# Optimization experiments

Hardware: AMD Instinct MI355X
Metric: run time of the kernel (lower is better)

The kernel has to match this reference:

```python
import jax, jax.numpy as jnp
import numpy as np
from jax import lax

SEQ_LEN = 64
B, H, E, V = 32, 512, 256, 32000


def setup_inputs() -> dict:
    key = jax.random.key(0)
    ks = jax.random.split(key, 8)
    return {
        "y0": jax.random.randint(ks[0], (B,), 0, V, dtype=jnp.int32),
        "h0": jax.random.normal(ks[1], (1, B, H), dtype=jnp.float32),
        "c0": jax.random.normal(ks[2], (1, B, H), dtype=jnp.float32),
        "emb": jax.random.normal(ks[3], (V, E), dtype=jnp.float32) * 0.02,
        "W_ih": jax.random.normal(ks[4], (4 * H, E + H), dtype=jnp.float32) * 0.02,
        "W_hh": jax.random.normal(ks[5], (4 * H, H), dtype=jnp.float32) * 0.02,
        "b_ih": jnp.zeros((4 * H,), dtype=jnp.float32),
        "b_hh": jnp.zeros((4 * H,), dtype=jnp.float32),
        "W_out": jax.random.normal(ks[6], (V, 2 * H + E), dtype=jnp.float32) * 0.02,
        "b_out": jnp.zeros((V,), dtype=jnp.float32),
    }


def reference(y0, h0, c0, emb, W_ih, W_hh, b_ih, b_hh, W_out, b_out):
    z = h0[0]  # (B, H) latent, reused at every step

    def step(carry, _):
        y, h, c = carry
        y_embed = emb[y]                                   # (B, E) embedding gather
        x = jnp.concatenate([z, y_embed], axis=1)          # (B, H+E)
        gates = x @ W_ih.T + b_ih + h @ W_hh.T + b_hh      # (B, 4H)
        i, f, g, o = jnp.split(gates, 4, axis=1)           # torch LSTM gate order
        i = jax.nn.sigmoid(i)
        f = jax.nn.sigmoid(f)
        g = jnp.tanh(g)
        o = jax.nn.sigmoid(o)
        c = f * c + i * g
        h = o * jnp.tanh(c)
        feat = jnp.concatenate([z, y_embed, h], axis=1)    # (B, 2H+E)
        logits = feat @ W_out.T + b_out                    # (B, V)
        y_next = jnp.argmax(logits, axis=-1).astype(jnp.int32)
        return (y_next, h, c), logits

    (_, _, _), logits = lax.scan(step, (y0, h0[0], c0[0]), None, length=SEQ_LEN)
    # logits: (T, B, V) -> torch.stack(outputs, dim=2) gives (B, V, T)
    return jnp.transpose(logits, (1, 2, 0))
```

## Files before the change

### kernel.cpp

```cpp
#include <hip/hip_runtime.h>
#include <cstdint>
#include <cstddef>

#define BB 32
#define HH 512
#define EE 256
#define VV 32000
#define TT 64
#define KDIM 1280
#define NBLK_V 500
#define WREG 2304
#define WTS  68

__device__ __forceinline__ float sigf(float x) { return 1.0f / (1.0f + expf(-x)); }

__global__ __launch_bounds__(256) void k_init(const float* __restrict__ h0,
                                              const float* __restrict__ c0,
                                              float* __restrict__ fA,
                                              float* __restrict__ fB,
                                              float* __restrict__ cA) {
    int idx = blockIdx.x * 256 + threadIdx.x;
    int kk = idx >> 5;
    int b  = idx & 31;
    float zv = h0[b * HH + kk];
    fA[kk * BB + b] = zv;
    fB[kk * BB + b] = zv;
    fA[(768 + kk) * BB + b] = zv;
    fB[(768 + kk) * BB + b] = zv;
    cA[b * HH + kk] = c0[b * HH + kk];
}

__global__ __launch_bounds__(256) void k_pre(const float* __restrict__ Wih,
                                             const float* __restrict__ bih,
                                             const float* __restrict__ bhh,
                                             const float* __restrict__ fz,
                                             float* __restrict__ gzT) {
    __shared__ float lds[4 * WREG];
    const int tid = threadIdx.x;
    const int l = tid & 63;
    const int wu = tid >> 6;
    const int j0 = blockIdx.x * 64;
    const int js = l & 15;
    const int bg = l >> 4;
    float* R = &lds[wu * WREG];

    float acc[4][8];
#pragma unroll
    for (int i = 0; i < 4; ++i)
#pragma unroll
        for (int q = 0; q < 8; ++q) acc[i][q] = 0.f;

    for (int ch = 0; ch < 4; ++ch) {
        int kg0 = wu * 128 + ch * 32;
#pragma unroll
        for (int i = 0; i < 8; ++i) {
            int f4 = i * 64 + l;
            int r = f4 >> 3;
            int c4 = (f4 & 7) * 4;
            float4 w = *(const float4*)&Wih[(size_t)(j0 + r) * 768 + kg0 + c4];
            R[(c4 + 0) * WTS + r] = w.x;
            R[(c4 + 1) * WTS + r] = w.y;
            R[(c4 + 2) * WTS + r] = w.z;
            R[(c4 + 3) * WTS + r] = w.w;
        }
#pragma unroll 4
        for (int kk = 0; kk < 32; ++kk) {
            float4 wv = *(const float4*)&R[kk * WTS + js * 4];
            const float* fp = &fz[(kg0 + kk) * BB + bg * 8];
            float4 fa = *(const float4*)fp;
            float4 fb = *(const float4*)(fp + 4);
            float w4[4] = {wv.x, wv.y, wv.z, wv.w};
            float f8[8] = {fa.x, fa.y, fa.z, fa.w, fb.x, fb.y, fb.z, fb.w};
#pragma unroll
            for (int i = 0; i < 4; ++i)
#pragma unroll
                for (int q = 0; q < 8; ++q) acc[i][q] = fmaf(w4[i], f8[q], acc[i][q]);
        }
    }
#pragma unroll
    for (int i = 0; i < 4; ++i) {
        int r = js * 4 + i;
        *(float4*)&R[r * 36 + bg * 8] = make_float4(acc[i][0], acc[i][1], acc[i][2], acc[i][3]);
        *(float4*)&R[r * 36 + bg * 8 + 4] = make_float4(acc[i][4], acc[i][5], acc[i][6], acc[i][7]);
    }
    __syncthreads();
    {
        int j = tid >> 2;
        int bq = (tid & 3) * 8;
        float bias = bih[j0 + j] + bhh[j0 + j];
#pragma unroll
        for (int q = 0; q < 8; ++q) {
            float s = lds[0 * WREG + j * 36 + bq + q] + lds[1 * WREG + j * 36 + bq + q] +
                      lds[2 * WREG + j * 36 + bq + q] + lds[3 * WREG + j * 36 + bq + q];
            gzT[(size_t)(j0 + j) * BB + bq + q] = s + bias;
        }
    }
}

__global__ __launch_bounds__(256) void k_prelog(
    const float* __restrict__ Wout, const float* __restrict__ bout,
    const float* __restrict__ fz, float* __restrict__ lzT) {
    __shared__ float lds[4 * WREG];
    const int tid = threadIdx.x;
    const int l = tid & 63;
    const int wu = tid >> 6;
    const int v0 = blockIdx.x * 64;
    const int vs = l & 15;
    const int bg = l >> 4;
    float* R = &lds[wu * WREG];

    float acc[4][8];
#pragma unroll
    for (int i = 0; i < 4; ++i)
#pragma unroll
        for (int q = 0; q < 8; ++q) acc[i][q] = 0.f;

    for (int ch = 0; ch < 4; ++ch) {
        int kg0 = wu * 128 + ch * 32;
#pragma unroll
        for (int i = 0; i < 8; ++i) {
            int f4 = i * 64 + l;
            int r = f4 >> 3;
            int c4 = (f4 & 7) * 4;
            float4 w = *(const float4*)&Wout[(size_t)(v0 + r) * KDIM + kg0 + c4];
            R[(c4 + 0) * WTS + r] = w.x;
            R[(c4 + 1) * WTS + r] = w.y;
            R[(c4 + 2) * WTS + r] = w.z;
            R[(c4 + 3) * WTS + r] = w.w;
        }
#pragma unroll 4
        for (int kk = 0; kk < 32; ++kk) {
            float4 wv = *(const float4*)&R[kk * WTS + vs * 4];
            const float* fp = &fz[(kg0 + kk) * BB + bg * 8];
            float4 fa = *(const float4*)fp;
            float4 fb = *(const float4*)(fp + 4);
            float w4[4] = {wv.x, wv.y, wv.z, wv.w};
            float f8[8] = {fa.x, fa.y, fa.z, fa.w, fb.x, fb.y, fb.z, fb.w};
#pragma unroll
            for (int i = 0; i < 4; ++i)
#pragma unroll
                for (int q = 0; q < 8; ++q) acc[i][q] = fmaf(w4[i], f8[q], acc[i][q]);
        }
    }
#pragma unroll
    for (int i = 0; i < 4; ++i) {
        int r = vs * 4 + i;
        *(float4*)&R[r * 36 + bg * 8] = make_float4(acc[i][0], acc[i][1], acc[i][2], acc[i][3]);
        *(float4*)&R[r * 36 + bg * 8 + 4] = make_float4(acc[i][4], acc[i][5], acc[i][6], acc[i][7]);
    }
    __syncthreads();
    {
        int b = tid >> 3;
        int rg = tid & 7;
#pragma unroll
        for (int i = 0; i < 8; ++i) {
            int r = i * 8 + rg;
            float s = lds[0 * WREG + r * 36 + b] + lds[1 * WREG + r * 36 + b] +
                      lds[2 * WREG + r * 36 + b] + lds[3 * WREG + r * 36 + b] +
                      bout[v0 + r];
            lzT[(size_t)(v0 + r) * BB + b] = s;
        }
    }
}

__global__ __launch_bounds__(256) void k_gates(
    int t, const int* __restrict__ y0, const float* __restrict__ emb,
    const float* __restrict__ Wih, const float* __restrict__ Whh,
    const float* __restrict__ gzT,
    const float* __restrict__ fCur, float* __restrict__ fNext,
    const float* __restrict__ cCur, float* __restrict__ cNext,
    const float* __restrict__ apv, const int* __restrict__ api) {
    __shared__ float lds[4 * WREG];
    const int tid = threadIdx.x;
    const int l = tid & 63;
    const int wu = tid >> 6;
    const int uc = blockIdx.x >> 2;
    const int bg4 = blockIdx.x & 3;
    const int b0 = bg4 * 8;
    const int js = l & 7;
    const int bg = l >> 3;
    const int rr = l >> 3;
    const int c4s = (l & 7) * 4;

    int yv0, yv1, yv2, yv3, yv4, yv5, yv6, yv7;
    if (t == 0) {
        yv0 = y0[b0 + 0]; yv1 = y0[b0 + 1]; yv2 = y0[b0 + 2]; yv3 = y0[b0 + 3];
        yv4 = y0[b0 + 4]; yv5 = y0[b0 + 5]; yv6 = y0[b0 + 6]; yv7 = y0[b0 + 7];
    } else {
        int bi = l >> 3;
        int e0 = l & 7;
        float best = -3.4e38f;
        int bidx = 0x7fffffff;
#pragma unroll 8
        for (int it = 0; it < 63; ++it) {
            int e = e0 + it * 8;
            if (e < NBLK_V) {
                float v = apv[(b0 + bi) * NBLK_V + e];
                int ix = api[(b0 + bi) * NBLK_V + e];
                if (v > best || (v == best && ix < bidx)) { best = v; bidx = ix; }
            }
        }
#pragma unroll
        for (int d = 1; d < 8; d <<= 1) {
            float ov = __shfl_xor(best, d, 8);
            int oi = __shfl_xor(bidx, d, 8);
            if (ov > best || (ov == best && oi < bidx)) { best = ov; bidx = oi; }
        }
        yv0 = __builtin_amdgcn_readlane(bidx, 0);
        yv1 = __builtin_amdgcn_readlane(bidx, 8);
        yv2 = __builtin_amdgcn_readlane(bidx, 16);
        yv3 = __builtin_amdgcn_readlane(bidx, 24);
        yv4 = __builtin_amdgcn_readlane(bidx, 32);
        yv5 = __builtin_amdgcn_readlane(bidx, 40);
        yv6 = __builtin_amdgcn_readlane(bidx, 48);
        yv7 = __builtin_amdgcn_readlane(bidx, 56);
    }
    int yA = (bg == 0) ? yv0 : (bg == 1) ? yv1 : (bg == 2) ? yv2 : (bg == 3) ? yv3
           : (bg == 4) ? yv4 : (bg == 5) ? yv5 : (bg == 6) ? yv6 : yv7;
    const float* embA = emb + (size_t)yA * EE;

    float acc[4];
#pragma unroll
    for (int i = 0; i < 4; ++i) acc[i] = 0.f;
    float* R = &lds[wu * WREG];

    float4 pw[4];
    {
        int kgp = wu * 192;
#pragma unroll
        for (int i = 0; i < 4; ++i) {
            int r = i * 8 + rr;
            int j = uc * 8 + (r & 7) + 512 * (r >> 3);
            pw[i] = (kgp < 256)
                ? *(const float4*)&Wih[(size_t)j * 768 + 512 + kgp + c4s]
                : *(const float4*)&Whh[(size_t)j * 512 + (kgp - 256) + c4s];
        }
    }

    for (int ch = 0; ch < 6; ++ch) {
        int kg0 = wu * 192 + ch * 32;
#pragma unroll
        for (int i = 0; i < 4; ++i) {
            int r = i * 8 + rr;
            R[(c4s + 0) * WTS + r] = pw[i].x;
            R[(c4s + 1) * WTS + r] = pw[i].y;
            R[(c4s + 2) * WTS + r] = pw[i].z;
            R[(c4s + 3) * WTS + r] = pw[i].w;
        }
        if (ch < 5) {
            int kg1 = kg0 + 32;
#pragma unroll
            for (int i = 0; i < 4; ++i) {
                int r = i * 8 + rr;
                int j = uc * 8 + (r & 7) + 512 * (r >> 3);
                pw[i] = (kg1 < 256)
                    ? *(const float4*)&Wih[(size_t)j * 768 + 512 + kg1 + c4s]
                    : *(const float4*)&Whh[(size_t)j * 512 + (kg1 - 256) + c4s];
            }
        }
        if (kg0 < 256) {
#pragma unroll 4
            for (int kk = 0; kk < 32; ++kk) {
                float4 wv = *(const float4*)&R[kk * WTS + js * 4];
                float f0 = embA[kg0 + kk];
                acc[0] = fmaf(wv.x, f0, acc[0]);
                acc[1] = fmaf(wv.y, f0, acc[1]);
                acc[2] = fmaf(wv.z, f0, acc[2]);
                acc[3] = fmaf(wv.w, f0, acc[3]);
            }
        } else {
#pragma unroll 4
            for (int kk = 0; kk < 32; ++kk) {
                float4 wv = *(const float4*)&R[kk * WTS + js * 4];
                float hv = fCur[(768 + kg0 - 256 + kk) * BB + b0 + bg];
                acc[0] = fmaf(wv.x, hv, acc[0]);
                acc[1] = fmaf(wv.y, hv, acc[1]);
                acc[2] = fmaf(wv.z, hv, acc[2]);
                acc[3] = fmaf(wv.w, hv, acc[3]);
            }
        }
    }
#pragma unroll
    for (int i = 0; i < 4; ++i) {
        int r = js * 4 + i;
        R[r * 9 + bg] = acc[i];
    }
    __syncthreads();

    if (tid < 64) {
        int u = tid & 7;
        int bl = tid >> 3;
        float pre[4];
#pragma unroll
        for (int g = 0; g < 4; ++g) {
            int r = u + 8 * g;
            float s = lds[0 * WREG + r * 9 + bl] + lds[1 * WREG + r * 9 + bl] +
                      lds[2 * WREG + r * 9 + bl] + lds[3 * WREG + r * 9 + bl];
            int j = uc * 8 + u + 512 * g;
            pre[g] = s + gzT[(size_t)j * BB + b0 + bl];
        }
        float ig = sigf(pre[0]);
        float fg = sigf(pre[1]);
        float gg = tanhf(pre[2]);
        float og = sigf(pre[3]);
        int u_g = uc * 8 + u;
        int b = b0 + bl;
        float cp = cCur[b * HH + u_g];
        float cn = fg * cp + ig * gg;
        float hn = og * tanhf(cn);
        cNext[b * HH + u_g] = cn;
        fNext[(768 + u_g) * BB + b] = hn;
    }
    if (uc == 0) {
        int yv[8] = {yv0, yv1, yv2, yv3, yv4, yv5, yv6, yv7};
#pragma unroll
        for (int i = 0; i < 8; ++i)
            fNext[(512 + tid) * BB + b0 + i] = emb[(size_t)yv[i] * EE + tid];
    }
}

__global__ __launch_bounds__(512, 4) void k_logits(
    int t, const float* __restrict__ Wout, const float* __restrict__ lzT,
    const float* __restrict__ feat, float* __restrict__ outbuf, int direct,
    float* __restrict__ apv, int* __restrict__ api) {
    __shared__ float lds[8 * WREG];
    const int tid = threadIdx.x;
    const int l = tid & 63;
    const int wu = tid >> 6;
    const int v0 = blockIdx.x * 64;
    const int vs = l & 15;
    const int bg = l >> 4;
    const int rr = l >> 3;
    const int c4s = (l & 7) * 4;
    float* R = &lds[wu * WREG];

    float acc[4][8];
#pragma unroll
    for (int i = 0; i < 4; ++i)
#pragma unroll
        for (int q = 0; q < 8; ++q) acc[i][q] = 0.f;

    float4 pw[8];
    {
        int kgp = wu * 96;
#pragma unroll
        for (int i = 0; i < 8; ++i)
            pw[i] = *(const float4*)&Wout[(size_t)(v0 + i * 8 + rr) * KDIM + 512 + kgp + c4s];
    }

    for (int ch = 0; ch < 3; ++ch) {
        int kg0 = wu * 96 + ch * 32;
#pragma unroll
        for (int i = 0; i < 8; ++i) {
            int r = i * 8 + rr;
            R[(c4s + 0) * WTS + r] = pw[i].x;
            R[(c4s + 1) * WTS + r] = pw[i].y;
            R[(c4s + 2) * WTS + r] = pw[i].z;
            R[(c4s + 3) * WTS + r] = pw[i].w;
        }
        if (ch < 2) {
            int kg1 = kg0 + 32;
#pragma unroll
            for (int i = 0; i < 8; ++i)
                pw[i] = *(const float4*)&Wout[(size_t)(v0 + i * 8 + rr) * KDIM + 512 + kg1 + c4s];
        }
#pragma unroll 4
        for (int kk = 0; kk < 32; ++kk) {
            float4 wv = *(const float4*)&R[kk * WTS + vs * 4];
            const float* fp = &feat[(512 + kg0 + kk) * BB + bg * 8];
            float4 fa = *(const float4*)fp;
            float4 fb = *(const float4*)(fp + 4);
            float w4[4] = {wv.x, wv.y, wv.z, wv.w};
            float f8[8] = {fa.x, fa.y, fa.z, fa.w, fb.x, fb.y, fb.z, fb.w};
#pragma unroll
            for (int i = 0; i < 4; ++i)
#pragma unroll
                for (int q = 0; q < 8; ++q) acc[i][q] = fmaf(w4[i], f8[q], acc[i][q]);
        }
    }
#pragma unroll
    for (int i = 0; i < 4; ++i) {
        int r = vs * 4 + i;
        *(float4*)&R[r * 36 + bg * 8] = make_float4(acc[i][0], acc[i][1], acc[i][2], acc[i][3]);
        *(float4*)&R[r * 36 + bg * 8 + 4] = make_float4(acc[i][4], acc[i][5], acc[i][6], acc[i][7]);
    }
    __syncthreads();

    {
        int b = tid >> 4;
        int rg = tid & 15;
        float best = -3.4e38f;
        int bidx = 0x7fffffff;
#pragma unroll
        for (int i = 0; i < 4; ++i) {
            int r = i * 16 + rg;
            float s = lds[0 * WREG + r * 36 + b] + lds[1 * WREG + r * 36 + b] +
                      lds[2 * WREG + r * 36 + b] + lds[3 * WREG + r * 36 + b] +
                      lds[4 * WREG + r * 36 + b] + lds[5 * WREG + r * 36 + b] +
                      lds[6 * WREG + r * 36 + b] + lds[7 * WREG + r * 36 + b] +
                      lzT[(size_t)(v0 + r) * BB + b];
            if (!direct)
                outbuf[((size_t)t * BB + b) * VV + v0 + r] = s;
            else
                outbuf[((size_t)b * VV + v0 + r) * TT + t] = s;
            if (s > best) { best = s; bidx = v0 + r; }
        }
#pragma unroll
        for (int d = 1; d < 16; d <<= 1) {
            float ov = __shfl_xor(best, d, 16);
            int oi = __shfl_xor(bidx, d, 16);
            if (ov > best || (ov == best && oi < bidx)) { best = ov; bidx = oi; }
        }
        if (rg == 0) {
            apv[b * NBLK_V + blockIdx.x] = best;
            api[b * NBLK_V + blockIdx.x] = bidx;
        }
    }
}

__global__ __launch_bounds__(256) void k_trans(const float* __restrict__ staged,
                                               float* __restrict__ out) {
    __shared__ float lds[64 * 65];
    int bx = blockIdx.x;
    int b = bx / NBLK_V;
    int v0 = (bx % NBLK_V) * 64;
    int tid = threadIdx.x;
    int vl = tid & 63;
    int tq = tid >> 6;
#pragma unroll
    for (int i = 0; i < 16; ++i) {
        int tt = tq * 16 + i;
        lds[tt * 65 + vl] = staged[((size_t)tt * BB + b) * VV + v0 + vl];
    }
    __syncthreads();
    int v2 = tid >> 2;
    int t0 = (tid & 3) * 16;
#pragma unroll
    for (int q = 0; q < 4; ++q) {
        float4 val;
        val.x = lds[(t0 + q * 4 + 0) * 65 + v2];
        val.y = lds[(t0 + q * 4 + 1) * 65 + v2];
        val.z = lds[(t0 + q * 4 + 2) * 65 + v2];
        val.w = lds[(t0 + q * 4 + 3) * 65 + v2];
        *(float4*)&out[((size_t)b * VV + v0 + v2) * TT + t0 + q * 4] = val;
    }
}

extern "C" void kernel_launch(void* const* d_in, const int* in_sizes, int n_in,
                              void* d_out, int out_size, void* d_ws, size_t ws_size,
                              hipStream_t stream) {
    const int* y0 = (const int*)d_in[0];
    const float* h0 = (const float*)d_in[1];
    const float* c0 = (const float*)d_in[2];
    const float* emb = (const float*)d_in[3];
    const float* Wih = (const float*)d_in[4];
    const float* Whh = (const float*)d_in[5];
    const float* bih = (const float*)d_in[6];
    const float* bhh = (const float*)d_in[7];
    const float* Wout = (const float*)d_in[8];
    const float* bout = (const float*)d_in[9];
    float* out = (float*)d_out;

    const size_t stagedFloats = (size_t)TT * BB * VV;
    const size_t smallBytes = (2 * (size_t)KDIM * BB + 2 * (size_t)BB * HH +
                               4 * HH * BB  + (size_t)BB * NBLK_V +
                               (size_t)VV * BB ) * 4 +
                              (size_t)BB * NBLK_V * sizeof(int) + 256;
    const size_t needStaged = stagedFloats * 4 + smallBytes;
    int use_staged = (ws_size >= needStaged) ? 1 : 0;

    char* w = (char*)d_ws;
    float* staged = (float*)w;
    size_t off = use_staged ? stagedFloats * 4 : 0;
    float* fA = (float*)(w + off); off += (size_t)KDIM * BB * 4;
    float* fB = (float*)(w + off); off += (size_t)KDIM * BB * 4;
    float* cA = (float*)(w + off); off += (size_t)BB * HH * 4;
    float* cB = (float*)(w + off); off += (size_t)BB * HH * 4;
    float* gzT = (float*)(w + off); off += (size_t)4 * HH * BB * 4;
    float* apv = (float*)(w + off); off += (size_t)BB * NBLK_V * 4;
    int* api = (int*)(w + off); off += (size_t)BB * NBLK_V * sizeof(int);
    float* lzT = (float*)(w + off);

    k_init<<<64, 256, 0, stream>>>(h0, c0, fA, fB, cA);
    k_pre<<<32, 256, 0, stream>>>(Wih, bih, bhh, fA, gzT);
    k_prelog<<<NBLK_V, 256, 0, stream>>>(Wout, bout, fA, lzT);

    for (int t = 0; t < TT; ++t) {
        const float* fCur = (t & 1) ? fB : fA;
        float* fNext = (t & 1) ? fA : fB;
        const float* cCur = (t & 1) ? cB : cA;
        float* cNext = (t & 1) ? cA : cB;
        k_gates<<<256, 256, 0, stream>>>(t, y0, emb, Wih, Whh, gzT,
                                         fCur, fNext, cCur, cNext, apv, api);
        k_logits<<<NBLK_V, 512, 0, stream>>>(t, Wout, lzT, fNext,
                                             use_staged ? staged : out,
                                             use_staged ? 0 : 1, apv, api);
    }
    if (use_staged) k_trans<<<BB * NBLK_V, 256, 0, stream>>>(staged, out);
}
```

Before: 5.265 ms.

## Fuse per-step gate and logits kernels into one persistent cooperative kernel

```diff
diff --git a/kernel.cpp b/kernel.cpp
--- a/kernel.cpp
+++ b/kernel.cpp
@@ -1,6 +1,9 @@
 #include <hip/hip_runtime.h>
+#include <hip/hip_cooperative_groups.h>
 #include <cstdint>
 #include <cstddef>
+
+namespace cg = cooperative_groups;
 
 #define BB 32
 #define HH 512
@@ -160,6 +163,275 @@
                       bout[v0 + r];
             lzT[(size_t)(v0 + r) * BB + b] = s;
         }
+    }
+}
+
+__global__ __launch_bounds__(512, 4) void k_fused(
+    const int* __restrict__ y0, const float* __restrict__ emb,
+    const float* __restrict__ Wih, const float* __restrict__ Whh,
+    const float* __restrict__ gzT,
+    float* __restrict__ fA, float* __restrict__ fB,
+    float* __restrict__ cA, float* __restrict__ cB,
+    const float* __restrict__ lzT, const float* __restrict__ Wout,
+    float* __restrict__ outbuf, int direct,
+    float* __restrict__ apv, int* __restrict__ api) {
+    cg::grid_group grid = cg::this_grid();
+    __shared__ float lds[8 * WREG];
+    const int blk = blockIdx.x;
+    const int tid = threadIdx.x;
+    const int l = tid & 63;
+    const int wu = tid >> 6;
+
+    for (int t = 0; t < TT; ++t) {
+        const float* fCur = (t & 1) ? fB : fA;
+        float* fNext = (t & 1) ? fA : fB;
+        const float* cCur = (t & 1) ? cB : cA;
+        float* cNext = (t & 1) ? cA : cB;
+
+        if (blk < 256) {
+            const int uc = blk >> 2;
+            const int bg4 = blk & 3;
+            const int b0 = bg4 * 8;
+            const int js = l & 7;
+            const int bgl = l >> 3;
+            const int rr = l >> 3;
+            const int c4s = (l & 7) * 4;
+
+            int yv0, yv1, yv2, yv3, yv4, yv5, yv6, yv7;
+            if (t == 0) {
+                yv0 = y0[b0 + 0]; yv1 = y0[b0 + 1]; yv2 = y0[b0 + 2]; yv3 = y0[b0 + 3];
+                yv4 = y0[b0 + 4]; yv5 = y0[b0 + 5]; yv6 = y0[b0 + 6]; yv7 = y0[b0 + 7];
+            } else {
+                int bi = l >> 3;
+                int e0 = l & 7;
+                float best = -3.4e38f;
+                int bidx = 0x7fffffff;
+#pragma unroll 8
+                for (int it = 0; it < 63; ++it) {
+                    int e = e0 + it * 8;
+                    if (e < NBLK_V) {
+                        float v = apv[(b0 + bi) * NBLK_V + e];
+                        int ix = api[(b0 + bi) * NBLK_V + e];
+                        if (v > best || (v == best && ix < bidx)) { best = v; bidx = ix; }
+                    }
+                }
+#pragma unroll
+                for (int d = 1; d < 8; d <<= 1) {
+                    float ov = __shfl_xor(best, d, 8);
+                    int oi = __shfl_xor(bidx, d, 8);
+                    if (ov > best || (ov == best && oi < bidx)) { best = ov; bidx = oi; }
+                }
+                yv0 = __builtin_amdgcn_readlane(bidx, 0);
+                yv1 = __builtin_amdgcn_readlane(bidx, 8);
+                yv2 = __builtin_amdgcn_readlane(bidx, 16);
+                yv3 = __builtin_amdgcn_readlane(bidx, 24);
+                yv4 = __builtin_amdgcn_readlane(bidx, 32);
+                yv5 = __builtin_amdgcn_readlane(bidx, 40);
+                yv6 = __builtin_amdgcn_readlane(bidx, 48);
+                yv7 = __builtin_amdgcn_readlane(bidx, 56);
+            }
+            int yA = (bgl == 0) ? yv0 : (bgl == 1) ? yv1 : (bgl == 2) ? yv2 : (bgl == 3) ? yv3
+                   : (bgl == 4) ? yv4 : (bgl == 5) ? yv5 : (bgl == 6) ? yv6 : yv7;
+            const float* embA = emb + (size_t)yA * EE;
+
+            float acc[4];
+#pragma unroll
+            for (int i = 0; i < 4; ++i) acc[i] = 0.f;
+            float* R = &lds[wu * WREG];
+
+            float4 pw[4];
+            {
+                int kgp = wu * 96;
+#pragma unroll
+                for (int i = 0; i < 4; ++i) {
+                    int r = i * 8 + rr;
+                    int j = uc * 8 + (r & 7) + 512 * (r >> 3);
+                    pw[i] = (kgp < 256)
+                        ? *(const float4*)&Wih[(size_t)j * 768 + 512 + kgp + c4s]
+                        : *(const float4*)&Whh[(size_t)j * 512 + (kgp - 256) + c4s];
+                }
+            }
+
+            for (int ch = 0; ch < 3; ++ch) {
+                int kg0 = wu * 96 + ch * 32;
+#pragma unroll
+                for (int i = 0; i < 4; ++i) {
+                    int r = i * 8 + rr;
+                    R[(c4s + 0) * WTS + r] = pw[i].x;
+                    R[(c4s + 1) * WTS + r] = pw[i].y;
+                    R[(c4s + 2) * WTS + r] = pw[i].z;
+                    R[(c4s + 3) * WTS + r] = pw[i].w;
+                }
+                if (ch < 2) {
+                    int kg1 = kg0 + 32;
+#pragma unroll
+                    for (int i = 0; i < 4; ++i) {
+                        int r = i * 8 + rr;
+                        int j = uc * 8 + (r & 7) + 512 * (r >> 3);
+                        pw[i] = (kg1 < 256)
+                            ? *(const float4*)&Wih[(size_t)j * 768 + 512 + kg1 + c4s]
+                            : *(const float4*)&Whh[(size_t)j * 512 + (kg1 - 256) + c4s];
+                    }
+                }
+                if (kg0 < 256) {
+#pragma unroll 4
+                    for (int kk = 0; kk < 32; ++kk) {
+                        float4 wv = *(const float4*)&R[kk * WTS + js * 4];
+                        float f0 = embA[kg0 + kk];
+                        acc[0] = fmaf(wv.x, f0, acc[0]);
+                        acc[1] = fmaf(wv.y, f0, acc[1]);
+                        acc[2] = fmaf(wv.z, f0, acc[2]);
+                        acc[3] = fmaf(wv.w, f0, acc[3]);
+                    }
+                } else {
+#pragma unroll 4
+                    for (int kk = 0; kk < 32; ++kk) {
+                        float4 wv = *(const float4*)&R[kk * WTS + js * 4];
+                        float hv = fCur[(768 + kg0 - 256 + kk) * BB + b0 + bgl];
+                        acc[0] = fmaf(wv.x, hv, acc[0]);
+                        acc[1] = fmaf(wv.y, hv, acc[1]);
+                        acc[2] = fmaf(wv.z, hv, acc[2]);
+                        acc[3] = fmaf(wv.w, hv, acc[3]);
+                    }
+                }
+            }
+#pragma unroll
+            for (int i = 0; i < 4; ++i) {
+                int r = js * 4 + i;
+                R[r * 9 + bgl] = acc[i];
+            }
+            __syncthreads();
+
+            if (tid < 64) {
+                int u = tid & 7;
+                int bl = tid >> 3;
+                float pre[4];
+#pragma unroll
+                for (int g = 0; g < 4; ++g) {
+                    int r = u + 8 * g;
+                    float s = 0.f;
+#pragma unroll
+                    for (int w8 = 0; w8 < 8; ++w8) s += lds[w8 * WREG + r * 9 + bl];
+                    int j = uc * 8 + u + 512 * g;
+                    pre[g] = s + gzT[(size_t)j * BB + b0 + bl];
+                }
+                float ig = sigf(pre[0]);
+                float fg = sigf(pre[1]);
+                float gg = tanhf(pre[2]);
+                float og = sigf(pre[3]);
+                int u_g = uc * 8 + u;
+                int b = b0 + bl;
+                float cp = cCur[b * HH + u_g];
+                float cn = fg * cp + ig * gg;
+                float hn = og * tanhf(cn);
+                cNext[b * HH + u_g] = cn;
+                fNext[(768 + u_g) * BB + b] = hn;
+            }
+            if (uc == 0 && tid < 256) {
+                int yv[8] = {yv0, yv1, yv2, yv3, yv4, yv5, yv6, yv7};
+#pragma unroll
+                for (int i = 0; i < 8; ++i)
+                    fNext[(512 + tid) * BB + b0 + i] = emb[(size_t)yv[i] * EE + tid];
+            }
+            __threadfence();
+        }
+        grid.sync();
+
+        if (blk < NBLK_V) {
+            const int v0 = blk * 64;
+            const int vs = l & 15;
+            const int bg = l >> 4;
+            const int rr = l >> 3;
+            const int c4s = (l & 7) * 4;
+            float* R = &lds[wu * WREG];
+
+            float acc[4][8];
+#pragma unroll
+            for (int i = 0; i < 4; ++i)
+#pragma unroll
+                for (int q = 0; q < 8; ++q) acc[i][q] = 0.f;
+
+            const float* feat = fNext;
+
+            float4 pw[8];
+            {
+                int kgp = wu * 96;
+#pragma unroll
+                for (int i = 0; i < 8; ++i)
+                    pw[i] = *(const float4*)&Wout[(size_t)(v0 + i * 8 + rr) * KDIM + 512 + kgp + c4s];
+            }
+
+            for (int ch = 0; ch < 3; ++ch) {
+                int kg0 = wu * 96 + ch * 32;
+#pragma unroll
+                for (int i = 0; i < 8; ++i) {
+                    int r = i * 8 + rr;
+                    R[(c4s + 0) * WTS + r] = pw[i].x;
+                    R[(c4s + 1) * WTS + r] = pw[i].y;
+                    R[(c4s + 2) * WTS + r] = pw[i].z;
+                    R[(c4s + 3) * WTS + r] = pw[i].w;
+                }
+                if (ch < 2) {
+                    int kg1 = kg0 + 32;
+#pragma unroll
+                    for (int i = 0; i < 8; ++i)
+                        pw[i] = *(const float4*)&Wout[(size_t)(v0 + i * 8 + rr) * KDIM + 512 + kg1 + c4s];
+                }
+#pragma unroll 4
+                for (int kk = 0; kk < 32; ++kk) {
+                    float4 wv = *(const float4*)&R[kk * WTS + vs * 4];
+                    const float* fp = &feat[(512 + kg0 + kk) * BB + bg * 8];
+                    float4 fa = *(const float4*)fp;
+                    float4 fb = *(const float4*)(fp + 4);
+                    float w4[4] = {wv.x, wv.y, wv.z, wv.w};
+                    float f8[8] = {fa.x, fa.y, fa.z, fa.w, fb.x, fb.y, fb.z, fb.w};
+#pragma unroll
+                    for (int i = 0; i < 4; ++i)
+#pragma unroll
+                        for (int q = 0; q < 8; ++q) acc[i][q] = fmaf(w4[i], f8[q], acc[i][q]);
+                }
+            }
+#pragma unroll
+            for (int i = 0; i < 4; ++i) {
+                int r = vs * 4 + i;
+                *(float4*)&R[r * 36 + bg * 8] = make_float4(acc[i][0], acc[i][1], acc[i][2], acc[i][3]);
+                *(float4*)&R[r * 36 + bg * 8 + 4] = make_float4(acc[i][4], acc[i][5], acc[i][6], acc[i][7]);
+            }
+            __syncthreads();
+
+            {
+                int b = tid >> 4;
+                int rg = tid & 15;
+                float best = -3.4e38f;
+                int bidx = 0x7fffffff;
+#pragma unroll
+                for (int i = 0; i < 4; ++i) {
+                    int r = i * 16 + rg;
+                    float s = lds[0 * WREG + r * 36 + b] + lds[1 * WREG + r * 36 + b] +
+                              lds[2 * WREG + r * 36 + b] + lds[3 * WREG + r * 36 + b] +
+                              lds[4 * WREG + r * 36 + b] + lds[5 * WREG + r * 36 + b] +
+                              lds[6 * WREG + r * 36 + b] + lds[7 * WREG + r * 36 + b] +
+                              lzT[(size_t)(v0 + r) * BB + b];
+                    if (!direct)
+                        outbuf[((size_t)t * BB + b) * VV + v0 + r] = s;
+                    else
+                        outbuf[((size_t)b * VV + v0 + r) * TT + t] = s;
+                    if (s > best) { best = s; bidx = v0 + r; }
+                }
+#pragma unroll
+                for (int d = 1; d < 16; d <<= 1) {
+                    float ov = __shfl_xor(best, d, 16);
+                    int oi = __shfl_xor(bidx, d, 16);
+                    if (ov > best || (ov == best && oi < bidx)) { best = ov; bidx = oi; }
+                }
+                if (rg == 0) {
+                    apv[b * NBLK_V + blk] = best;
+                    api[b * NBLK_V + blk] = bidx;
+                }
+            }
+            __threadfence();
+        }
+        grid.sync();
     }
 }
 
@@ -485,16 +757,40 @@
     k_pre<<<32, 256, 0, stream>>>(Wih, bih, bhh, fA, gzT);
     k_prelog<<<NBLK_V, 256, 0, stream>>>(Wout, bout, fA, lzT);
 
-    for (int t = 0; t < TT; ++t) {
-        const float* fCur = (t & 1) ? fB : fA;
-        float* fNext = (t & 1) ? fA : fB;
-        const float* cCur = (t & 1) ? cB : cA;
-        float* cNext = (t & 1) ? cA : cB;
-        k_gates<<<256, 256, 0, stream>>>(t, y0, emb, Wih, Whh, gzT,
-                                         fCur, fNext, cCur, cNext, apv, api);
-        k_logits<<<NBLK_V, 512, 0, stream>>>(t, Wout, lzT, fNext,
-                                             use_staged ? staged : out,
-                                             use_staged ? 0 : 1, apv, api);
+    float* outptr = use_staged ? staged : out;
+    int direct = use_staged ? 0 : 1;
+
+    int dev = 0;
+    hipGetDevice(&dev);
+    int coopAttr = 0;
+    hipDeviceGetAttribute(&coopAttr, hipDeviceAttributeCooperativeLaunch, dev);
+    int maxb = 0;
+    hipOccupancyMaxActiveBlocksPerMultiprocessor(&maxb, k_fused, 512, 0);
+
+    bool done = false;
+    if (coopAttr && maxb >= 2) {
+        void* kargs[] = {
+            (void*)&y0, (void*)&emb, (void*)&Wih, (void*)&Whh, (void*)&gzT,
+            (void*)&fA, (void*)&fB, (void*)&cA, (void*)&cB,
+            (void*)&lzT, (void*)&Wout, (void*)&outptr, (void*)&direct,
+            (void*)&apv, (void*)&api};
+        hipError_t e = hipLaunchCooperativeKernel((const void*)k_fused,
+                                                  dim3(NBLK_V), dim3(512),
+                                                  kargs, 0, stream);
+        done = (e == hipSuccess);
+    }
+
+    if (!done) {
+        for (int t = 0; t < TT; ++t) {
+            const float* fCur = (t & 1) ? fB : fA;
+            float* fNext = (t & 1) ? fA : fB;
+            const float* cCur = (t & 1) ? cB : cA;
+            float* cNext = (t & 1) ? cA : cB;
+            k_gates<<<256, 256, 0, stream>>>(t, y0, emb, Wih, Whh, gzT,
+                                             fCur, fNext, cCur, cNext, apv, api);
+            k_logits<<<NBLK_V, 512, 0, stream>>>(t, Wout, lzT, fNext,
+                                                 outptr, direct, apv, api);
+        }
     }
     if (use_staged) k_trans<<<BB * NBLK_V, 256, 0, stream>>>(staged, out);
 }
```

Result: no change. 5.265 ms (+0.0%).

## Split LSTM gate kernel finer and add row-major h buffer with register prefetch

Applied to the files above, without the earlier changes.

```diff
diff --git a/kernel.cpp b/kernel.cpp
--- a/kernel.cpp
+++ b/kernel.cpp
@@ -18,7 +18,8 @@
                                               const float* __restrict__ c0,
                                               float* __restrict__ fA,
                                               float* __restrict__ fB,
-                                              float* __restrict__ cA) {
+                                              float* __restrict__ cA,
+                                              float* __restrict__ hA) {
     int idx = blockIdx.x * 256 + threadIdx.x;
     int kk = idx >> 5;
     int b  = idx & 31;
@@ -28,6 +29,7 @@
     fA[(768 + kk) * BB + b] = zv;
     fB[(768 + kk) * BB + b] = zv;
     cA[b * HH + kk] = c0[b * HH + kk];
+    hA[b * HH + kk] = zv;
 }
 
 __global__ __launch_bounds__(256) void k_pre(const float* __restrict__ Wih,
@@ -163,11 +165,12 @@
     }
 }
 
-__global__ __launch_bounds__(256) void k_gates(
+__global__ __launch_bounds__(256, 2) void k_gates(
     int t, const int* __restrict__ y0, const float* __restrict__ emb,
     const float* __restrict__ Wih, const float* __restrict__ Whh,
     const float* __restrict__ gzT,
-    const float* __restrict__ fCur, float* __restrict__ fNext,
+    const float* __restrict__ hCur, float* __restrict__ hNext,
+    float* __restrict__ fNext,
     const float* __restrict__ cCur, float* __restrict__ cNext,
     const float* __restrict__ apv, const int* __restrict__ api) {
     __shared__ float lds[4 * WREG];
@@ -178,7 +181,7 @@
     const int bg4 = blockIdx.x & 3;
     const int b0 = bg4 * 8;
     const int js = l & 7;
-    const int bg = l >> 3;
+    const int bgl = l >> 3;
     const int rr = l >> 3;
     const int c4s = (l & 7) * 4;
 
@@ -215,101 +218,95 @@
         yv6 = __builtin_amdgcn_readlane(bidx, 48);
         yv7 = __builtin_amdgcn_readlane(bidx, 56);
     }
-    int yA = (bg == 0) ? yv0 : (bg == 1) ? yv1 : (bg == 2) ? yv2 : (bg == 3) ? yv3
-           : (bg == 4) ? yv4 : (bg == 5) ? yv5 : (bg == 6) ? yv6 : yv7;
+    int yA = (bgl == 0) ? yv0 : (bgl == 1) ? yv1 : (bgl == 2) ? yv2 : (bgl == 3) ? yv3
+           : (bgl == 4) ? yv4 : (bgl == 5) ? yv5 : (bgl == 6) ? yv6 : yv7;
     const float* embA = emb + (size_t)yA * EE;
-
-    float acc[4];
-#pragma unroll
-    for (int i = 0; i < 4; ++i) acc[i] = 0.f;
+    const float* hRow = hCur + (size_t)(b0 + bgl) * HH;
+
+    float acc[2] = {0.f, 0.f};
     float* R = &lds[wu * WREG];
 
-    float4 pw[4];
+    float4 pw[3][2];
+    float4 pe[3][8];
+
+#define GATES_LOAD(set, kg)                                                      \
+    {                                                                            \
+        const int kg_ = (kg);                                                    \
+        _Pragma("unroll")                                                        \
+        for (int i = 0; i < 2; ++i) {                                            \
+            int r = i * 8 + rr;                                                  \
+            int j = uc * 4 + (r & 3) + 512 * (r >> 2);                           \
+            pw[set][i] = (kg_ < 256)                                             \
+                ? *(const float4*)&Wih[(size_t)j * 768 + 512 + kg_ + c4s]        \
+                : *(const float4*)&Whh[(size_t)j * 512 + (kg_ - 256) + c4s];     \
+        }                                                                        \
+        const float* xp_ = (kg_ < 256) ? (embA + kg_) : (hRow + (kg_ - 256));    \
+        _Pragma("unroll")                                                        \
+        for (int i = 0; i < 8; ++i) pe[set][i] = *(const float4*)(xp_ + i * 4);  \
+    }
+
     {
         int kgp = wu * 192;
-#pragma unroll
-        for (int i = 0; i < 4; ++i) {
+        GATES_LOAD(0, kgp)
+        GATES_LOAD(1, kgp + 32)
+    }
+
+#pragma unroll
+    for (int ch = 0; ch < 6; ++ch) {
+        const int set = ch % 3;
+#pragma unroll
+        for (int i = 0; i < 2; ++i) {
             int r = i * 8 + rr;
-            int j = uc * 8 + (r & 7) + 512 * (r >> 3);
-            pw[i] = (kgp < 256)
-                ? *(const float4*)&Wih[(size_t)j * 768 + 512 + kgp + c4s]
-                : *(const float4*)&Whh[(size_t)j * 512 + (kgp - 256) + c4s];
-        }
-    }
-
-    for (int ch = 0; ch < 6; ++ch) {
-        int kg0 = wu * 192 + ch * 32;
-#pragma unroll
-        for (int i = 0; i < 4; ++i) {
-            int r = i * 8 + rr;
-            R[(c4s + 0) * WTS + r] = pw[i].x;
-            R[(c4s + 1) * WTS + r] = pw[i].y;
-            R[(c4s + 2) * WTS + r] = pw[i].z;
-            R[(c4s + 3) * WTS + r] = pw[i].w;
-        }
-        if (ch < 5) {
-            int kg1 = kg0 + 32;
-#pragma unroll
-            for (int i = 0; i < 4; ++i) {
-                int r = i * 8 + rr;
-                int j = uc * 8 + (r & 7) + 512 * (r >> 3);
-                pw[i] = (kg1 < 256)
-                    ? *(const float4*)&Wih[(size_t)j * 768 + 512 + kg1 + c4s]
-                    : *(const float4*)&Whh[(size_t)j * 512 + (kg1 - 256) + c4s];
-            }
-        }
-        if (kg0 < 256) {
-#pragma unroll 4
-            for (int kk = 0; kk < 32; ++kk) {
-                float4 wv = *(const float4*)&R[kk * WTS + js * 4];
-                float f0 = embA[kg0 + kk];
-                acc[0] = fmaf(wv.x, f0, acc[0]);
-                acc[1] = fmaf(wv.y, f0, acc[1]);
-                acc[2] = fmaf(wv.z, f0, acc[2]);
-                acc[3] = fmaf(wv.w, f0, acc[3]);
-            }
-        } else {
-#pragma unroll 4
-            for (int kk = 0; kk < 32; ++kk) {
-                float4 wv = *(const float4*)&R[kk * WTS + js * 4];
-                float hv = fCur[(768 + kg0 - 256 + kk) * BB + b0 + bg];
-                acc[0] = fmaf(wv.x, hv, acc[0]);
-                acc[1] = fmaf(wv.y, hv, acc[1]);
-                acc[2] = fmaf(wv.z, hv, acc[2]);
-                acc[3] = fmaf(wv.w, hv, acc[3]);
-            }
-        }
-    }
-#pragma unroll
-    for (int i = 0; i < 4; ++i) {
-        int r = js * 4 + i;
-        R[r * 9 + bg] = acc[i];
+            R[(c4s + 0) * WTS + r] = pw[set][i].x;
+            R[(c4s + 1) * WTS + r] = pw[set][i].y;
+            R[(c4s + 2) * WTS + r] = pw[set][i].z;
+            R[(c4s + 3) * WTS + r] = pw[set][i].w;
+        }
+        if (ch < 4) {
+            int kg2 = wu * 192 + (ch + 2) * 32;
+            GATES_LOAD((ch + 2) % 3, kg2)
+        }
+#pragma unroll
+        for (int kk = 0; kk < 32; ++kk) {
+            float2 wv = *(const float2*)&R[kk * WTS + js * 2];
+            float xv = ((const float*)&pe[set][0])[kk];
+            acc[0] = fmaf(wv.x, xv, acc[0]);
+            acc[1] = fmaf(wv.y, xv, acc[1]);
+        }
+    }
+#undef GATES_LOAD
+
+#pragma unroll
+    for (int i = 0; i < 2; ++i) {
+        int r = js * 2 + i;
+        R[r * 9 + bgl] = acc[i];
     }
     __syncthreads();
 
-    if (tid < 64) {
-        int u = tid & 7;
-        int bl = tid >> 3;
+    if (tid < 32) {
+        int u = tid & 3;
+        int bl = tid >> 2;
         float pre[4];
 #pragma unroll
         for (int g = 0; g < 4; ++g) {
-            int r = u + 8 * g;
+            int r = g * 4 + u;
             float s = lds[0 * WREG + r * 9 + bl] + lds[1 * WREG + r * 9 + bl] +
                       lds[2 * WREG + r * 9 + bl] + lds[3 * WREG + r * 9 + bl];
-            int j = uc * 8 + u + 512 * g;
+            int j = uc * 4 + u + 512 * g;
             pre[g] = s + gzT[(size_t)j * BB + b0 + bl];
         }
         float ig = sigf(pre[0]);
         float fg = sigf(pre[1]);
         float gg = tanhf(pre[2]);
         float og = sigf(pre[3]);
-        int u_g = uc * 8 + u;
+        int u_g = uc * 4 + u;
         int b = b0 + bl;
         float cp = cCur[b * HH + u_g];
         float cn = fg * cp + ig * gg;
         float hn = og * tanhf(cn);
         cNext[b * HH + u_g] = cn;
         fNext[(768 + u_g) * BB + b] = hn;
+        hNext[(size_t)b * HH + u_g] = hn;
     }
     if (uc == 0) {
         int yv[8] = {yv0, yv1, yv2, yv3, yv4, yv5, yv6, yv7};
@@ -462,7 +459,7 @@
     float* out = (float*)d_out;
 
     const size_t stagedFloats = (size_t)TT * BB * VV;
-    const size_t smallBytes = (2 * (size_t)KDIM * BB + 2 * (size_t)BB * HH +
+    const size_t smallBytes = (2 * (size_t)KDIM * BB + 4 * (size_t)BB * HH +
                                4 * HH * BB  + (size_t)BB * NBLK_V +
                                (size_t)VV * BB ) * 4 +
                               (size_t)BB * NBLK_V * sizeof(int) + 256;
@@ -476,25 +473,30 @@
     float* fB = (float*)(w + off); off += (size_t)KDIM * BB * 4;
     float* cA = (float*)(w + off); off += (size_t)BB * HH * 4;
     float* cB = (float*)(w + off); off += (size_t)BB * HH * 4;
+    float* hA = (float*)(w + off); off += (size_t)BB * HH * 4;
+    float* hB = (float*)(w + off); off += (size_t)BB * HH * 4;
     float* gzT = (float*)(w + off); off += (size_t)4 * HH * BB * 4;
     float* apv = (float*)(w + off); off += (size_t)BB * NBLK_V * 4;
     int* api = (int*)(w + off); off += (size_t)BB * NBLK_V * sizeof(int);
     float* lzT = (float*)(w + off);
 
-    k_init<<<64, 256, 0, stream>>>(h0, c0, fA, fB, cA);
+    k_init<<<64, 256, 0, stream>>>(h0, c0, fA, fB, cA, hA);
     k_pre<<<32, 256, 0, stream>>>(Wih, bih, bhh, fA, gzT);
     k_prelog<<<NBLK_V, 256, 0, stream>>>(Wout, bout, fA, lzT);
 
+    float* outptr = use_staged ? staged : out;
+    int direct = use_staged ? 0 : 1;
+
     for (int t = 0; t < TT; ++t) {
-        const float* fCur = (t & 1) ? fB : fA;
         float* fNext = (t & 1) ? fA : fB;
         const float* cCur = (t & 1) ? cB : cA;
         float* cNext = (t & 1) ? cA : cB;
-        k_gates<<<256, 256, 0, stream>>>(t, y0, emb, Wih, Whh, gzT,
-                                         fCur, fNext, cCur, cNext, apv, api);
+        const float* hCur = (t & 1) ? hB : hA;
+        float* hNext = (t & 1) ? hA : hB;
+        k_gates<<<512, 256, 0, stream>>>(t, y0, emb, Wih, Whh, gzT,
+                                         hCur, hNext, fNext, cCur, cNext, apv, api);
         k_logits<<<NBLK_V, 512, 0, stream>>>(t, Wout, lzT, fNext,
-                                             use_staged ? staged : out,
-                                             use_staged ? 0 : 1, apv, api);
+                                             outptr, direct, apv, api);
     }
     if (use_staged) k_trans<<<BB * NBLK_V, 256, 0, stream>>>(staged, out);
 }
```

Result: slower. 6.555 ms (+24.5%).
